# Performance work log

Hardware: AMD Instinct MI355X
Metric: run time of the kernel (lower is better)

## Reference

```python
import jax, jax.numpy as jnp
import numpy as np
import math

HEAD_SIZE = 64
WHERE_CONST = -10000.0


def setup_inputs() -> dict:
    key = jax.random.key(0)
    k1, k2, k3 = jax.random.split(key, 3)
    shape = (4, 16, 2048, 64)  # [B, H, S, D]
    q = jax.random.normal(k1, shape, dtype=jnp.float32)
    k = jax.random.normal(k2, shape, dtype=jnp.float32)
    v = jax.random.normal(k3, shape, dtype=jnp.float32)
    return {"q": q, "k": k, "v": v}


def reference(q, k, v):
    # scores: [B, H, Sq, Sk]
    scale = 1.0 / math.sqrt(HEAD_SIZE)
    scores = jnp.einsum('bhqd,bhkd->bhqk', q, k) * scale
    q_len, k_len = q.shape[-2], k.shape[-2]
    causal_mask = jnp.tril(jnp.ones((q_len, k_len), dtype=bool))[None, None]
    scores = jnp.where(causal_mask, scores, WHERE_CONST)
    probs = jax.nn.softmax(scores, axis=-1)
    # dropout rate is 0.0 -> identity
    out = jnp.einsum('bhqk,bhkd->bhqd', probs, v)  # [B, H, S, D]
    out = jnp.swapaxes(out, 1, 2)                  # [B, S, H, D]
    B, S, H, D = out.shape
    return out.reshape(B, S, H * D)
```

## Files before the change

### kernel.cpp

```cpp
#include <hip/hip_runtime.h>
#include <hip/hip_bf16.h>

typedef __bf16 bf16x8_t __attribute__((ext_vector_type(8)));
typedef float  f32x4_t  __attribute__((ext_vector_type(4)));
typedef short  short8_t __attribute__((ext_vector_type(8)));
typedef short  short4_t __attribute__((ext_vector_type(4)));

#define NB   4
#define NH   16
#define SEQ  2048
#define HD   64
#define BQ   64
#define BKV  64
#define LSTR 72

#define MASK2 (-14426.950408889634f)
#define QSCL  (0.18033688011112042f)

__device__ __forceinline__ int swz(int rowi, int blk) {
    return rowi * LSTR + (((blk) ^ (rowi >> 3)) & 7) * 8;
}

__global__ void __launch_bounds__(256)
fa_fwd(const float* __restrict__ qg,
       const float* __restrict__ kg,
       const float* __restrict__ vg,
       float* __restrict__ outg) {
    __shared__ alignas(16) short k_lds[BKV * LSTR];
    __shared__ alignas(16) short vt_lds[HD * LSTR];
    __shared__ alignas(16) short p_lds[BQ * LSTR];

    const int tid  = threadIdx.x;
    const int wave = tid >> 6;
    const int lane = tid & 63;
    const int l16  = lane & 15;
    const int quad = lane >> 4;

    const int bh = blockIdx.x;
    const int qt = (int)gridDim.y - 1 - (int)blockIdx.y;
    const int q0 = qt * BQ;

    const size_t base = (size_t)bh * SEQ * HD;
    const float* qp = qg + base;
    const float* kp = kg + base;
    const float* vp = vg + base;

    bf16x8_t qf0, qf1;
    {
        const float* qr = qp + (size_t)(q0 + wave * 16 + l16) * HD;
        f32x4_t qa = *(const f32x4_t*)(qr + quad * 8);
        f32x4_t qb = *(const f32x4_t*)(qr + quad * 8 + 4);
        f32x4_t qc = *(const f32x4_t*)(qr + 32 + quad * 8);
        f32x4_t qd = *(const f32x4_t*)(qr + 32 + quad * 8 + 4);
        #pragma unroll
        for (int j = 0; j < 4; ++j) {
            qf0[j]     = (__bf16)(qa[j] * QSCL);
            qf0[4 + j] = (__bf16)(qb[j] * QSCL);
            qf1[j]     = (__bf16)(qc[j] * QSCL);
            qf1[4 + j] = (__bf16)(qd[j] * QSCL);
        }
    }

    f32x4_t o_acc[4];
    const f32x4_t zero4 = {0.0f, 0.0f, 0.0f, 0.0f};
    #pragma unroll
    for (int c = 0; c < 4; ++c) o_acc[c] = zero4;
    float m_r[4], l_r[4];
    #pragma unroll
    for (int r = 0; r < 4; ++r) { m_r[r] = MASK2; l_r[r] = 0.0f; }

    const int srow = tid >> 4;
    const int cb   = tid & 15;
    const int d0   = cb * 4;

    f32x4_t kreg[4], vreg[4];

    auto issue = [&](int kt0) {
        const float* kr = kp + (size_t)kt0 * HD + d0;
        const float* vr = vp + (size_t)kt0 * HD + d0;
        #pragma unroll
        for (int it = 0; it < 4; ++it) {
            const size_t off = (size_t)(it * 16 + srow) * HD;
            kreg[it] = *(const f32x4_t*)(kr + off);
            vreg[it] = *(const f32x4_t*)(vr + off);
        }
    };

    auto stage = [&]() {
        #pragma unroll
        for (int it = 0; it < 4; ++it) {
            const int r0 = it * 16 + srow;
            short4_t kw;
            #pragma unroll
            for (int j = 0; j < 4; ++j) kw[j] = __builtin_bit_cast(short, (__bf16)kreg[it][j]);
            *(short4_t*)&k_lds[swz(r0, cb >> 1) + (d0 & 7)] = kw;
            #pragma unroll
            for (int j = 0; j < 4; ++j)
                vt_lds[swz(d0 + j, r0 >> 3) + (r0 & 7)] = __builtin_bit_cast(short, (__bf16)vreg[it][j]);
        }
    };

    issue(0);

    const int ntiles = qt + 1;
    for (int t = 0; t < ntiles; ++t) {
        const int kt0 = t * BKV;
        __syncthreads();
        stage();
        __syncthreads();
        if (t + 1 < ntiles) issue(kt0 + BKV);

        f32x4_t s_acc[4];
        #pragma unroll
        for (int c = 0; c < 4; ++c) s_acc[c] = zero4;
        #pragma unroll
        for (int c = 0; c < 4; ++c) {
            const int kvrow = c * 16 + l16;
            bf16x8_t b0 = __builtin_bit_cast(bf16x8_t, *(const short8_t*)&k_lds[swz(kvrow, quad)]);
            bf16x8_t b1 = __builtin_bit_cast(bf16x8_t, *(const short8_t*)&k_lds[swz(kvrow, quad + 4)]);
            s_acc[c] = __builtin_amdgcn_mfma_f32_16x16x32_bf16(qf0, b0, s_acc[c], 0, 0, 0);
            s_acc[c] = __builtin_amdgcn_mfma_f32_16x16x32_bf16(qf1, b1, s_acc[c], 0, 0, 0);
        }

        float sv[4][4];
        float vmax[4] = {MASK2, MASK2, MASK2, MASK2};
        const bool diag = (kt0 == q0);
        #pragma unroll
        for (int c = 0; c < 4; ++c) {
            #pragma unroll
            for (int r = 0; r < 4; ++r) {
                float x = s_acc[c][r];
                if (diag) {
                    int col = c * 16 + l16;
                    int row = wave * 16 + quad * 4 + r;
                    if (col > row) x = MASK2;
                }
                sv[c][r] = x;
                vmax[r] = fmaxf(vmax[r], x);
            }
        }
        #pragma unroll
        for (int r = 0; r < 4; ++r) {
            vmax[r] = fmaxf(vmax[r], __shfl_xor(vmax[r], 1));
            vmax[r] = fmaxf(vmax[r], __shfl_xor(vmax[r], 2));
            vmax[r] = fmaxf(vmax[r], __shfl_xor(vmax[r], 4));
            vmax[r] = fmaxf(vmax[r], __shfl_xor(vmax[r], 8));
        }

        bool grow = (vmax[0] > m_r[0]) | (vmax[1] > m_r[1]) |
                    (vmax[2] > m_r[2]) | (vmax[3] > m_r[3]);
        if (__any((int)grow)) {
            #pragma unroll
            for (int r = 0; r < 4; ++r) {
                float mn = fmaxf(m_r[r], vmax[r]);
                float a  = __builtin_amdgcn_exp2f(m_r[r] - mn);
                m_r[r] = mn;
                l_r[r] *= a;
                #pragma unroll
                for (int c = 0; c < 4; ++c) o_acc[c][r] *= a;
            }
        }

        float rs[4] = {0.0f, 0.0f, 0.0f, 0.0f};
        #pragma unroll
        for (int c = 0; c < 4; ++c) {
            #pragma unroll
            for (int r = 0; r < 4; ++r) {
                float p = __builtin_amdgcn_exp2f(sv[c][r] - m_r[r]);
                rs[r] += p;
                int prow = wave * 16 + quad * 4 + r;
                p_lds[swz(prow, 2 * c + (l16 >> 3)) + (l16 & 7)] =
                    __builtin_bit_cast(short, (__bf16)p);
            }
        }
        #pragma unroll
        for (int r = 0; r < 4; ++r) {
            rs[r] += __shfl_xor(rs[r], 1);
            rs[r] += __shfl_xor(rs[r], 2);
            rs[r] += __shfl_xor(rs[r], 4);
            rs[r] += __shfl_xor(rs[r], 8);
            l_r[r] += rs[r];
        }


        const int prow = wave * 16 + l16;
        bf16x8_t pf0 = __builtin_bit_cast(bf16x8_t, *(const short8_t*)&p_lds[swz(prow, quad)]);
        bf16x8_t pf1 = __builtin_bit_cast(bf16x8_t, *(const short8_t*)&p_lds[swz(prow, quad + 4)]);
        #pragma unroll
        for (int c = 0; c < 4; ++c) {
            const int d = c * 16 + l16;
            bf16x8_t b0 = __builtin_bit_cast(bf16x8_t, *(const short8_t*)&vt_lds[swz(d, quad)]);
            bf16x8_t b1 = __builtin_bit_cast(bf16x8_t, *(const short8_t*)&vt_lds[swz(d, quad + 4)]);
            o_acc[c] = __builtin_amdgcn_mfma_f32_16x16x32_bf16(pf0, b0, o_acc[c], 0, 0, 0);
            o_acc[c] = __builtin_amdgcn_mfma_f32_16x16x32_bf16(pf1, b1, o_acc[c], 0, 0, 0);
        }
    }

    const int b = bh >> 4;
    const int h = bh & 15;
    #pragma unroll
    for (int r = 0; r < 4; ++r) {
        const int row = q0 + wave * 16 + quad * 4 + r;
        const float inv_l = 1.0f / fmaxf(l_r[r], 1e-30f);
        float* op = outg + ((size_t)b * SEQ + row) * (NH * HD) + h * HD;
        #pragma unroll
        for (int c = 0; c < 4; ++c) {
            float val = o_acc[c][r] * inv_l;
            unsigned bits = __builtin_bit_cast(unsigned, val);
            if ((bits & 0x7F800000u) == 0x7F800000u) val = 0.0f;
            op[c * 16 + l16] = val;
        }
    }
}

extern "C" void kernel_launch(void* const* d_in, const int* in_sizes, int n_in,
                              void* d_out, int out_size, void* d_ws, size_t ws_size,
                              hipStream_t stream) {
    const float* q = (const float*)d_in[0];
    const float* k = (const float*)d_in[1];
    const float* v = (const float*)d_in[2];
    float* out = (float*)d_out;
    dim3 grid(NB * NH, SEQ / BQ);
    fa_fwd<<<grid, 256, 0, stream>>>(q, k, v, out);
}
```

Before: 232.9 us.

## Compute transposed scores so each lane owns one query row in softmax

After: 191.8 us. 1.21x faster.

```diff
diff --git a/kernel.cpp b/kernel.cpp
--- a/kernel.cpp
+++ b/kernel.cpp
@@ -65,38 +65,39 @@
     const f32x4_t zero4 = {0.0f, 0.0f, 0.0f, 0.0f};
     #pragma unroll
     for (int c = 0; c < 4; ++c) o_acc[c] = zero4;
-    float m_r[4], l_r[4];
-    #pragma unroll
-    for (int r = 0; r < 4; ++r) { m_r[r] = MASK2; l_r[r] = 0.0f; }
-
-    const int srow = tid >> 4;
-    const int cb   = tid & 15;
-    const int d0   = cb * 4;
+    float m_x = MASK2, l_x = 0.0f;
+
+    const int sr = tid >> 4;
+    const int cb = tid & 15;
+    const int d0 = cb * 4;
 
     f32x4_t kreg[4], vreg[4];
 
     auto issue = [&](int kt0) {
-        const float* kr = kp + (size_t)kt0 * HD + d0;
-        const float* vr = vp + (size_t)kt0 * HD + d0;
-        #pragma unroll
-        for (int it = 0; it < 4; ++it) {
-            const size_t off = (size_t)(it * 16 + srow) * HD;
-            kreg[it] = *(const f32x4_t*)(kr + off);
-            vreg[it] = *(const f32x4_t*)(vr + off);
+        const float* kr = kp + (size_t)(kt0 + 4 * sr) * HD + d0;
+        const float* vr = vp + (size_t)(kt0 + 4 * sr) * HD + d0;
+        #pragma unroll
+        for (int i = 0; i < 4; ++i) {
+            kreg[i] = *(const f32x4_t*)(kr + i * HD);
+            vreg[i] = *(const f32x4_t*)(vr + i * HD);
         }
     };
 
     auto stage = [&]() {
         #pragma unroll
-        for (int it = 0; it < 4; ++it) {
-            const int r0 = it * 16 + srow;
+        for (int i = 0; i < 4; ++i) {
+            const int r0 = 4 * sr + i;
             short4_t kw;
             #pragma unroll
-            for (int j = 0; j < 4; ++j) kw[j] = __builtin_bit_cast(short, (__bf16)kreg[it][j]);
-            *(short4_t*)&k_lds[swz(r0, cb >> 1) + (d0 & 7)] = kw;
-            #pragma unroll
-            for (int j = 0; j < 4; ++j)
-                vt_lds[swz(d0 + j, r0 >> 3) + (r0 & 7)] = __builtin_bit_cast(short, (__bf16)vreg[it][j]);
+            for (int j = 0; j < 4; ++j) kw[j] = __builtin_bit_cast(short, (__bf16)kreg[i][j]);
+            *(short4_t*)&k_lds[swz(r0, cb >> 1) + (cb & 1) * 4] = kw;
+        }
+        #pragma unroll
+        for (int j = 0; j < 4; ++j) {
+            short4_t vw;
+            #pragma unroll
+            for (int i = 0; i < 4; ++i) vw[i] = __builtin_bit_cast(short, (__bf16)vreg[i][j]);
+            *(short4_t*)&vt_lds[swz(d0 + j, sr >> 1) + (sr & 1) * 4] = vw;
         }
     };
 
@@ -113,79 +114,71 @@
         f32x4_t s_acc[4];
         #pragma unroll
         for (int c = 0; c < 4; ++c) s_acc[c] = zero4;
+        __builtin_amdgcn_s_setprio(1);
         #pragma unroll
         for (int c = 0; c < 4; ++c) {
             const int kvrow = c * 16 + l16;
-            bf16x8_t b0 = __builtin_bit_cast(bf16x8_t, *(const short8_t*)&k_lds[swz(kvrow, quad)]);
-            bf16x8_t b1 = __builtin_bit_cast(bf16x8_t, *(const short8_t*)&k_lds[swz(kvrow, quad + 4)]);
-            s_acc[c] = __builtin_amdgcn_mfma_f32_16x16x32_bf16(qf0, b0, s_acc[c], 0, 0, 0);
-            s_acc[c] = __builtin_amdgcn_mfma_f32_16x16x32_bf16(qf1, b1, s_acc[c], 0, 0, 0);
-        }
+            bf16x8_t kf0 = __builtin_bit_cast(bf16x8_t, *(const short8_t*)&k_lds[swz(kvrow, quad)]);
+            bf16x8_t kf1 = __builtin_bit_cast(bf16x8_t, *(const short8_t*)&k_lds[swz(kvrow, quad + 4)]);
+            s_acc[c] = __builtin_amdgcn_mfma_f32_16x16x32_bf16(kf0, qf0, s_acc[c], 0, 0, 0);
+            s_acc[c] = __builtin_amdgcn_mfma_f32_16x16x32_bf16(kf1, qf1, s_acc[c], 0, 0, 0);
+        }
+        __builtin_amdgcn_s_setprio(0);
 
         float sv[4][4];
-        float vmax[4] = {MASK2, MASK2, MASK2, MASK2};
+        float vmax = MASK2;
         const bool diag = (kt0 == q0);
+        const int qloc = wave * 16 + l16;
         #pragma unroll
         for (int c = 0; c < 4; ++c) {
             #pragma unroll
             for (int r = 0; r < 4; ++r) {
                 float x = s_acc[c][r];
-                if (diag) {
-                    int col = c * 16 + l16;
-                    int row = wave * 16 + quad * 4 + r;
-                    if (col > row) x = MASK2;
-                }
+                if (diag && (c * 16 + quad * 4 + r > qloc)) x = MASK2;
                 sv[c][r] = x;
-                vmax[r] = fmaxf(vmax[r], x);
+                vmax = fmaxf(vmax, x);
             }
         }
-        #pragma unroll
-        for (int r = 0; r < 4; ++r) {
-            vmax[r] = fmaxf(vmax[r], __shfl_xor(vmax[r], 1));
-            vmax[r] = fmaxf(vmax[r], __shfl_xor(vmax[r], 2));
-            vmax[r] = fmaxf(vmax[r], __shfl_xor(vmax[r], 4));
-            vmax[r] = fmaxf(vmax[r], __shfl_xor(vmax[r], 8));
-        }
-
-        bool grow = (vmax[0] > m_r[0]) | (vmax[1] > m_r[1]) |
-                    (vmax[2] > m_r[2]) | (vmax[3] > m_r[3]);
-        if (__any((int)grow)) {
+        vmax = fmaxf(vmax, __shfl_xor(vmax, 16));
+        vmax = fmaxf(vmax, __shfl_xor(vmax, 32));
+
+        if (__any((int)(vmax > m_x))) {
+            float mn = fmaxf(m_x, vmax);
+            float a  = __builtin_amdgcn_exp2f(m_x - mn);
+            m_x = mn;
+            l_x *= a;
+            float ar[4];
+            #pragma unroll
+            for (int r = 0; r < 4; ++r)
+                ar[r] = __shfl(a, (lane & 48) | (quad * 4 + r));
+            #pragma unroll
+            for (int c = 0; c < 4; ++c)
+                #pragma unroll
+                for (int r = 0; r < 4; ++r)
+                    o_acc[c][r] *= ar[r];
+        }
+
+        const int prow = wave * 16 + l16;
+        float rs = 0.0f;
+        #pragma unroll
+        for (int c = 0; c < 4; ++c) {
+            short4_t pw;
             #pragma unroll
             for (int r = 0; r < 4; ++r) {
-                float mn = fmaxf(m_r[r], vmax[r]);
-                float a  = __builtin_amdgcn_exp2f(m_r[r] - mn);
-                m_r[r] = mn;
-                l_r[r] *= a;
-                #pragma unroll
-                for (int c = 0; c < 4; ++c) o_acc[c][r] *= a;
+                float p = __builtin_amdgcn_exp2f(sv[c][r] - m_x);
+                rs += p;
+                pw[r] = __builtin_bit_cast(short, (__bf16)p);
             }
-        }
-
-        float rs[4] = {0.0f, 0.0f, 0.0f, 0.0f};
-        #pragma unroll
-        for (int c = 0; c < 4; ++c) {
-            #pragma unroll
-            for (int r = 0; r < 4; ++r) {
-                float p = __builtin_amdgcn_exp2f(sv[c][r] - m_r[r]);
-                rs[r] += p;
-                int prow = wave * 16 + quad * 4 + r;
-                p_lds[swz(prow, 2 * c + (l16 >> 3)) + (l16 & 7)] =
-                    __builtin_bit_cast(short, (__bf16)p);
-            }
-        }
-        #pragma unroll
-        for (int r = 0; r < 4; ++r) {
-            rs[r] += __shfl_xor(rs[r], 1);
-            rs[r] += __shfl_xor(rs[r], 2);
-            rs[r] += __shfl_xor(rs[r], 4);
-            rs[r] += __shfl_xor(rs[r], 8);
-            l_r[r] += rs[r];
-        }
-
-
-        const int prow = wave * 16 + l16;
+            *(short4_t*)&p_lds[swz(prow, 2 * c + (quad >> 1)) + (quad & 1) * 4] = pw;
+        }
+        rs += __shfl_xor(rs, 16);
+        rs += __shfl_xor(rs, 32);
+        l_x += rs;
+
+
         bf16x8_t pf0 = __builtin_bit_cast(bf16x8_t, *(const short8_t*)&p_lds[swz(prow, quad)]);
         bf16x8_t pf1 = __builtin_bit_cast(bf16x8_t, *(const short8_t*)&p_lds[swz(prow, quad + 4)]);
+        __builtin_amdgcn_s_setprio(1);
         #pragma unroll
         for (int c = 0; c < 4; ++c) {
             const int d = c * 16 + l16;
@@ -194,14 +187,16 @@
             o_acc[c] = __builtin_amdgcn_mfma_f32_16x16x32_bf16(pf0, b0, o_acc[c], 0, 0, 0);
             o_acc[c] = __builtin_amdgcn_mfma_f32_16x16x32_bf16(pf1, b1, o_acc[c], 0, 0, 0);
         }
+        __builtin_amdgcn_s_setprio(0);
     }
 
     const int b = bh >> 4;
     const int h = bh & 15;
     #pragma unroll
     for (int r = 0; r < 4; ++r) {
+        const float lr = __shfl(l_x, (lane & 48) | (quad * 4 + r));
+        const float inv_l = 1.0f / fmaxf(lr, 1e-30f);
         const int row = q0 + wave * 16 + quad * 4 + r;
-        const float inv_l = 1.0f / fmaxf(l_r[r], 1e-30f);
         float* op = outg + ((size_t)b * SEQ + row) * (NH * HD) + h * HD;
         #pragma unroll
         for (int c = 0; c < 4; ++c) {
```
